# Kernel tuning notes

Hardware: AMD Instinct MI355X
Metric: run time of the kernel (lower is better)

Reference implementation:

```python
import jax, jax.numpy as jnp
import numpy as np

GAMMAK = 1.0 / 256.0  # 1/(2*d) so kernel values don't underflow for unit-gaussian data


def setup_inputs() -> dict:
    key = jax.random.key(0)
    k1, k2, k3, k4, k5 = jax.random.split(key, 5)
    N, d = 8192, 128
    X = jax.random.normal(k1, (N, d), dtype=jnp.float32)
    y = jax.random.normal(k2, (N - 1, d), dtype=jnp.float32)
    y_next = jax.random.normal(k3, (N - 1, d), dtype=jnp.float32)
    # reset_transform initializes R=eye, t=0; perturb slightly for nontrivial math
    R = jnp.eye(d, dtype=jnp.float32) + 0.01 * jax.random.normal(k4, (d, d), dtype=jnp.float32)
    t = 0.01 * jax.random.normal(k5, (d, 1), dtype=jnp.float32)
    return {"X": X, "y": y, "y_next": y_next, "R": R, "t": t}


def reference(X, y, y_next, R, t):
    # _transform_pts: (R @ y.T + t).T == y @ R.T + t.squeeze()
    yt = y @ R.T + t[:, 0]            # (N-1, d)
    Xb = X[:-1]                        # (N-1, d) kernel base points
    # pairwise_sqeuclidean(Xb, yt), clamped at 0
    sq = jnp.clip(
        jnp.sum(Xb * Xb, axis=1)[:, None]
        + jnp.sum(yt * yt, axis=1)[None, :]
        - 2.0 * (Xb @ yt.T),
        0.0, None,
    )                                  # (N-1, N-1)
    G = jnp.exp(-GAMMAK * sq)
    # diag(1/rowsum) @ G  ==  G / rowsum[:, None]  (avoids explicit NxN diagonal)
    y_pred = (G / jnp.sum(G, axis=1, keepdims=True)) @ X[1:]  # (N-1, d)
    return y_pred
```

## Files before the change

### kernel.cpp

```cpp
#include <hip/hip_runtime.h>
#include <hip/hip_bf16.h>


#define LOG2E 1.44269504088896340736f
#define KNEG (-(1.0f/256.0f)*LOG2E)
#define KA2C (2.0f*(1.0f/256.0f)*LOG2E)

typedef __attribute__((ext_vector_type(4)))  float f32x4;
typedef __attribute__((ext_vector_type(16))) float f32x16;
typedef __attribute__((ext_vector_type(8)))  short bf16x8;

__device__ __forceinline__ unsigned short f2bf(float f) {
  unsigned u = __builtin_bit_cast(unsigned, f);
  u = (u + 0x7fffu + ((u >> 16) & 1u)) >> 16;
  return (unsigned short)u;
}
__device__ __forceinline__ unsigned pk2bf(float a, float b) {
  __hip_bfloat162 h = __float22bfloat162_rn(float2{a, b});
  unsigned u;
  __builtin_memcpy(&u, &h, 4);
  return u;
}
__device__ __forceinline__ bf16x8 pack8(float4 p0, float4 p1) {
  uint4 u;
  u.x = pk2bf(p0.x, p0.y); u.y = pk2bf(p0.z, p0.w);
  u.z = pk2bf(p1.x, p1.y); u.w = pk2bf(p1.z, p1.w);
  return __builtin_bit_cast(bf16x8, u);
}
__device__ __forceinline__ float fast_exp2(float x) {
#if __has_builtin(__builtin_amdgcn_exp2f)
  return __builtin_amdgcn_exp2f(x);
#else
  return exp2f(x);
#endif
}
__device__ __forceinline__ void gl2lds16(const void* g, void* l) {
  __builtin_amdgcn_global_load_lds((const __attribute__((address_space(1))) unsigned int*)g,
                                   (__attribute__((address_space(3))) unsigned int*)l, 16, 0, 0);
}
__device__ __forceinline__ f32x16 mfma_32x32x16(bf16x8 a, bf16x8 b, f32x16 c) {
  return __builtin_amdgcn_mfma_f32_32x32x16_bf16(a, b, c, 0, 0, 0);
}

#define T32S  16384
#define V32O  8192

__global__ __launch_bounds__(256) void k_prep(const float* __restrict__ y,
                                              const float* __restrict__ R,
                                              const float* __restrict__ t,
                                              const float* __restrict__ X,
                                              unsigned short* __restrict__ ctp,
                                              float* __restrict__ ynp) {
  __shared__ union {
    unsigned short ytt[128 * 132];
    float xt[65 * 132];
  } sm;
  const int tid = threadIdx.x;

  if (blockIdx.x < 64) {
    const int wv = tid >> 6, ln = tid & 63;
    const int l = ln & 31, h = ln >> 5;
    const int B = blockIdx.x;
    const int rw = B * 128 + wv * 32;

    bf16x8 af[8];
    {
      int row = rw + l; if (row > 8190) row = 8190;
      const float* yr = y + (size_t)row * 128;
#pragma unroll
      for (int kc = 0; kc < 8; ++kc) {
        float4 p0 = *(const float4*)(yr + kc*16 + 8*h);
        float4 p1 = *(const float4*)(yr + kc*16 + 8*h + 4);
        af[kc] = pack8(p0, p1);
      }
    }
    f32x16 acc[4];
#pragma unroll
    for (int cc=0; cc<4; ++cc)
#pragma unroll
      for (int i=0;i<16;++i) acc[cc][i] = 0.f;
#pragma unroll
    for (int cc=0; cc<4; ++cc) {
      const float* Rr = R + (size_t)(cc*32 + l) * 128;
#pragma unroll
      for (int kc=0; kc<8; ++kc) {
        float4 p0 = *(const float4*)(Rr + kc*16 + 8*h);
        float4 p1 = *(const float4*)(Rr + kc*16 + 8*h + 4);
        acc[cc] = mfma_32x32x16(af[kc], pack8(p0, p1), acc[cc]);
      }
    }
    float tv0 = t[l], tv1 = t[32+l], tv2 = t[64+l], tv3 = t[96+l];
    float v0[16], v1[16], v2[16], v3[16], ssq[16];
#pragma unroll
    for (int r=0;r<16;++r) {
      v0[r]=acc[0][r]+tv0; v1[r]=acc[1][r]+tv1; v2[r]=acc[2][r]+tv2; v3[r]=acc[3][r]+tv3;
      ssq[r] = v0[r]*v0[r] + v1[r]*v1[r] + v2[r]*v2[r] + v3[r]*v3[r];
    }
#pragma unroll
    for (int off=1; off<32; off<<=1)
#pragma unroll
      for (int r=0;r<16;++r) ssq[r] += __shfl_xor(ssq[r], off, 64);
    if (l < 16) {
      int r = l;
      int grow = rw + (r&3) + 8*(r>>2) + 4*h;
      ynp[grow] = (grow >= 8191) ? -1.0e30f : KNEG * ssq[r];
    }
#pragma unroll
    for (int r=0;r<16;++r) {
      int rloc = wv*32 + (r&3) + 8*(r>>2) + 4*h;
      sm.ytt[rloc*132 +   0 + l] = f2bf(KA2C * v0[r]);
      sm.ytt[rloc*132 +  32 + l] = f2bf(KA2C * v1[r]);
      sm.ytt[rloc*132 +  64 + l] = f2bf(KA2C * v2[r]);
      sm.ytt[rloc*132 +  96 + l] = f2bf(KA2C * v3[r]);
    }
    __syncthreads();
    const int Tt = B*4 + wv;
    char* base = (char*)ctp + (size_t)Tt*T32S;
#pragma unroll
    for (int kc=0;kc<8;++kc) {
      const unsigned short* s = &sm.ytt[(wv*32 + l)*132 + kc*16 + 8*h];
      uint2 a = *(const uint2*)(s);
      uint2 b = *(const uint2*)(s + 4);
      uint4 o; o.x=a.x; o.y=a.y; o.z=b.x; o.w=b.y;
      *(uint4*)(base + kc*1024 + ln*16) = o;
    }
  } else {
    const int T = blockIdx.x - 64;
    const int jt = T * 64;
    {
      int rr = tid >> 2, q4 = tid & 3;
      int row = jt + rr; if (row > 8191) row = 8191;
      const float* src = X + (size_t)row*128 + q4*32;
      float* dst = &sm.xt[rr*132 + q4*32];
#pragma unroll
      for (int i=0;i<8;++i) *(float4*)(dst + i*4) = *(const float4*)(src + i*4);
      if (tid < 4) {
        int row2 = jt + 64; if (row2 > 8191) row2 = 8191;
        const float* s2 = X + (size_t)row2*128 + tid*32;
        float* d2 = &sm.xt[64*132 + tid*32];
#pragma unroll
        for (int i=0;i<8;++i) *(float4*)(d2 + i*4) = *(const float4*)(s2 + i*4);
      }
    }
    __syncthreads();
#pragma unroll
    for (int it=0; it<4; ++it) {
      int E = tid + it*256;
      int lp = E & 63, grp = E >> 6;
      int cc = grp & 3, jc16 = grp >> 2;
      int jb = jc16*16 + 8*(lp>>5);
      int c  = cc*32 + (lp & 31);
      uint4 o;
      o.x = pk2bf(sm.xt[(jb+1)*132 + c], sm.xt[(jb+2)*132 + c]);
      o.y = pk2bf(sm.xt[(jb+3)*132 + c], sm.xt[(jb+4)*132 + c]);
      o.z = pk2bf(sm.xt[(jb+5)*132 + c], sm.xt[(jb+6)*132 + c]);
      o.w = pk2bf(sm.xt[(jb+7)*132 + c], sm.xt[(jb+8)*132 + c]);
      int t32 = T*2 + (jc16 >> 1);
      int chunk = (jc16 & 1)*4 + cc;
      *(uint4*)((char*)ctp + (size_t)t32*T32S + V32O + chunk*1024 + lp*16) = o;
    }
  }
}

__global__ __launch_bounds__(256, 3) void k_main(
    const float* __restrict__ X,
    const unsigned short* __restrict__ ctp,
    const float* __restrict__ ynp,
    float* __restrict__ accp,
    float* __restrict__ rsp,
    int js) {
  __shared__ unsigned short stg[2][T32S/2];
  __shared__ unsigned short gls[4*32*68];
  const int tid = threadIdx.x;
  const int wv = tid >> 6, ln = tid & 63;
  const int l = ln & 31, h = ln >> 5;
  const int row = blockIdx.x*128 + wv*32 + l;

  bf16x8 qf[8];
  {
    const float* xr = X + (size_t)row * 128;
#pragma unroll
    for (int kc=0;kc<8;++kc) {
      float4 p0 = *(const float4*)(xr + kc*16 + 8*h);
      float4 p1 = *(const float4*)(xr + kc*16 + 8*h + 4);
      qf[kc] = pack8(p0, p1);
    }
  }
  f32x16 acc[4];
#pragma unroll
  for (int cc=0;cc<4;++cc)
#pragma unroll
    for (int i=0;i<16;++i) acc[cc][i]=0.f;
  float rs = 0.f;
  const int sp = blockIdx.y;
  const int Tbeg = (sp * 256) / js;
  const int Tend = ((sp + 1) * 256) / js;

  {
    const char* cb = (const char*)ctp + (size_t)Tbeg*T32S;
#pragma unroll
    for (int i=0;i<4;++i) {
      int c = wv*4 + i;
      gl2lds16(cb + c*1024 + ln*16, (char*)stg[0] + c*1024);
    }
  }
  int cur = 0;
  for (int T = Tbeg; T < Tend; ++T) {
    __syncthreads();
    if (T + 1 < Tend) {
      const char* cb = (const char*)ctp + (size_t)(T+1)*T32S;
#pragma unroll
      for (int i=0;i<4;++i) {
        int c = wv*4 + i;
        gl2lds16(cb + c*1024 + ln*16, (char*)stg[cur^1] + c*1024);
      }
    }
    const char* yb = (const char*)stg[cur];
    const char* vb = (const char*)stg[cur] + V32O;
    f32x4 yv[4];
#pragma unroll
    for (int rg=0;rg<4;++rg)
      yv[rg] = *(const f32x4*)(ynp + T*32 + 8*rg + 4*h);
    f32x16 s0, s1;
#pragma unroll
    for (int i=0;i<16;++i) { s0[i]=0.f; s1[i]=0.f; }
#pragma unroll
    for (int kc=0;kc<4;++kc) {
      bf16x8 a0 = *(const bf16x8*)(yb + (2*kc  )*1024 + ln*16);
      bf16x8 a1 = *(const bf16x8*)(yb + (2*kc+1)*1024 + ln*16);
      s0 = mfma_32x32x16(a0, qf[2*kc  ], s0);
      s1 = mfma_32x32x16(a1, qf[2*kc+1], s1);
    }
#pragma unroll
    for (int rg=0;rg<4;++rg) {
      float g0 = fast_exp2(s0[rg*4+0] + s1[rg*4+0] + yv[rg][0]);
      float g1 = fast_exp2(s0[rg*4+1] + s1[rg*4+1] + yv[rg][1]);
      float g2 = fast_exp2(s0[rg*4+2] + s1[rg*4+2] + yv[rg][2]);
      float g3 = fast_exp2(s0[rg*4+3] + s1[rg*4+3] + yv[rg][3]);
      rs += (g0+g1) + (g2+g3);
      uint2 w; w.x = pk2bf(g0, g1); w.y = pk2bf(g2, g3);
      int j0 = 8*rg + 4*h;
      *(uint2*)&gls[(wv*32+l)*68 + j0] = w;
    }
    __builtin_amdgcn_wave_barrier();
#pragma unroll
    for (int jj=0; jj<2; ++jj) {
      const unsigned short* gp = &gls[(wv*32+l)*68 + jj*16 + 8*h];
      uint2 g0 = *(const uint2*)(gp);
      uint2 g1 = *(const uint2*)(gp + 4);
      uint4 gv; gv.x=g0.x; gv.y=g0.y; gv.z=g1.x; gv.w=g1.y;
      bf16x8 pb = __builtin_bit_cast(bf16x8, gv);
#pragma unroll
      for (int cc=0;cc<4;++cc) {
        bf16x8 a2 = *(const bf16x8*)(vb + (jj*4+cc)*1024 + ln*16);
        acc[cc] = mfma_32x32x16(a2, pb, acc[cc]);
      }
    }
    __builtin_amdgcn_wave_barrier();
    cur ^= 1;
  }
  rs += __shfl_xor(rs, 32, 64);
  if (h == 0) rsp[(size_t)sp*8192 + row] = rs;
#pragma unroll
  for (int cc=0;cc<4;++cc)
#pragma unroll
    for (int r=0;r<16;++r) {
      int c = cc*32 + (r&3) + 8*(r>>2) + 4*h;
      accp[((size_t)sp*128 + c)*8192 + row] = acc[cc][r];
    }
}

__global__ __launch_bounds__(256) void k_fin(const float* __restrict__ accp,
                                             const float* __restrict__ rsp,
                                             float* __restrict__ out,
                                             int js) {
  __shared__ float tr[64*68];
  __shared__ float rinv[64];
  const int tid = threadIdx.x;
  const int r0 = blockIdx.x * 64;
  const int c0 = blockIdx.y * 64;
  if (tid < 64) {
    float s = 0.f;
    for (int sp=0; sp<js; ++sp) s += rsp[(size_t)sp*8192 + r0 + tid];
    rinv[tid] = 1.f / s;
  }
  const int rq = tid & 15, cg = tid >> 4;
  float v[4][4];
#pragma unroll
  for (int cc=0;cc<4;++cc)
#pragma unroll
    for (int k=0;k<4;++k) v[cc][k]=0.f;
  for (int sp=0; sp<js; ++sp) {
    const float* base = accp + ((size_t)sp*128 + c0 + cg*4)*8192 + r0 + rq*4;
#pragma unroll
    for (int cc=0; cc<4; ++cc) {
      float4 p = *(const float4*)(base + (size_t)cc*8192);
      v[cc][0]+=p.x; v[cc][1]+=p.y; v[cc][2]+=p.z; v[cc][3]+=p.w;
    }
  }
  __syncthreads();
#pragma unroll
  for (int cc=0;cc<4;++cc)
#pragma unroll
    for (int k=0;k<4;++k)
      tr[(rq*4+k)*68 + cg*4+cc] = v[cc][k] * rinv[rq*4+k];
  __syncthreads();
  {
    int r = tid >> 2, q = tid & 3;
    int grow = r0 + r;
    if (grow < 8191) {
      float* dst = out + (size_t)grow*128 + c0 + q*16;
      const float* s2 = &tr[r*68 + q*16];
#pragma unroll
      for (int i=0;i<4;++i) *(float4*)(dst + i*4) = *(const float4*)(s2 + i*4);
    }
  }
}

extern "C" void kernel_launch(void* const* d_in, const int* in_sizes, int n_in,
                              void* d_out, int out_size, void* d_ws, size_t ws_size,
                              hipStream_t stream) {
  const float* X = (const float*)d_in[0];
  const float* y = (const float*)d_in[1];
  const float* R = (const float*)d_in[3];
  const float* t = (const float*)d_in[4];
  float* out = (float*)d_out;
  char* ws = (char*)d_ws;

  unsigned short* ctp = (unsigned short*)ws;
  size_t ynoff = (size_t)256 * T32S;
  float* ynp = (float*)(ws + ynoff);
  size_t rspoff = ynoff + 32*1024;
  float* rsp  = (float*)(ws + rspoff);
  size_t accoff = rspoff + 512*1024;
  float* accp = (float*)(ws + accoff);

  int js = 12;
  while (js > 1 && accoff + (size_t)js*128*8192*4 > ws_size) js >>= 1;

  k_prep<<<dim3(192), dim3(256), 0, stream>>>(y, R, t, X, ctp, ynp);
  k_main<<<dim3(64, js), dim3(256), 0, stream>>>(X, ctp, ynp, accp, rsp, js);
  k_fin<<<dim3(128, 2), dim3(256), 0, stream>>>(accp, rsp, out, js);
}
```

Measured before the change: 139.7 us.

## Process two 32-row query groups per wave to reuse staged Y/V tiles

Each wave now holds query fragments and accumulators for two 32-row groups, 128 rows apart. Every LDS-staged Y and V fragment feeds two MFMAs instead of one, which halves LDS and global tile traffic per output row. The two score accumulators, which used to split the K dimension, now belong to separate row groups. The grid shrinks to 32 row blocks, the column split goes from 12 to 16, and the occupancy hint drops from 3 to 2 blocks per CU to make room for the doubled register and LDS footprint. The risks are fewer resident waves to hide latency and a longer MFMA dependency chain per accumulator.

```diff
diff --git a/kernel.cpp b/kernel.cpp
--- a/kernel.cpp
+++ b/kernel.cpp
@@ -162,7 +162,7 @@
   }
 }
 
-__global__ __launch_bounds__(256, 3) void k_main(
+__global__ __launch_bounds__(256, 2) void k_main(
     const float* __restrict__ X,
     const unsigned short* __restrict__ ctp,
     const float* __restrict__ ynp,
@@ -170,28 +170,31 @@
     float* __restrict__ rsp,
     int js) {
   __shared__ unsigned short stg[2][T32S/2];
-  __shared__ unsigned short gls[4*32*68];
+  __shared__ unsigned short gls[2*4*32*68];
   const int tid = threadIdx.x;
   const int wv = tid >> 6, ln = tid & 63;
   const int l = ln & 31, h = ln >> 5;
-  const int row = blockIdx.x*128 + wv*32 + l;
-
-  bf16x8 qf[8];
-  {
-    const float* xr = X + (size_t)row * 128;
+  const int rbase = blockIdx.x*256 + wv*32;
+
+  bf16x8 qf[2][8];
+#pragma unroll
+  for (int g=0; g<2; ++g) {
+    const float* xr = X + (size_t)(rbase + g*128 + l) * 128;
 #pragma unroll
     for (int kc=0;kc<8;++kc) {
       float4 p0 = *(const float4*)(xr + kc*16 + 8*h);
       float4 p1 = *(const float4*)(xr + kc*16 + 8*h + 4);
-      qf[kc] = pack8(p0, p1);
-    }
-  }
-  f32x16 acc[4];
-#pragma unroll
-  for (int cc=0;cc<4;++cc)
-#pragma unroll
-    for (int i=0;i<16;++i) acc[cc][i]=0.f;
-  float rs = 0.f;
+      qf[g][kc] = pack8(p0, p1);
+    }
+  }
+  f32x16 acc[2][4];
+#pragma unroll
+  for (int g=0;g<2;++g)
+#pragma unroll
+    for (int cc=0;cc<4;++cc)
+#pragma unroll
+      for (int i=0;i<16;++i) acc[g][cc][i]=0.f;
+  float rs0 = 0.f, rs1 = 0.f;
   const int sp = blockIdx.y;
   const int Tbeg = (sp * 256) / js;
   const int Tend = ((sp + 1) * 256) / js;
@@ -217,57 +220,73 @@
     }
     const char* yb = (const char*)stg[cur];
     const char* vb = (const char*)stg[cur] + V32O;
-    f32x4 yv[4];
-#pragma unroll
-    for (int rg=0;rg<4;++rg)
-      yv[rg] = *(const f32x4*)(ynp + T*32 + 8*rg + 4*h);
     f32x16 s0, s1;
 #pragma unroll
     for (int i=0;i<16;++i) { s0[i]=0.f; s1[i]=0.f; }
 #pragma unroll
-    for (int kc=0;kc<4;++kc) {
-      bf16x8 a0 = *(const bf16x8*)(yb + (2*kc  )*1024 + ln*16);
-      bf16x8 a1 = *(const bf16x8*)(yb + (2*kc+1)*1024 + ln*16);
-      s0 = mfma_32x32x16(a0, qf[2*kc  ], s0);
-      s1 = mfma_32x32x16(a1, qf[2*kc+1], s1);
+    for (int kc=0;kc<8;++kc) {
+      bf16x8 a = *(const bf16x8*)(yb + kc*1024 + ln*16);
+      s0 = mfma_32x32x16(a, qf[0][kc], s0);
+      s1 = mfma_32x32x16(a, qf[1][kc], s1);
     }
 #pragma unroll
     for (int rg=0;rg<4;++rg) {
-      float g0 = fast_exp2(s0[rg*4+0] + s1[rg*4+0] + yv[rg][0]);
-      float g1 = fast_exp2(s0[rg*4+1] + s1[rg*4+1] + yv[rg][1]);
-      float g2 = fast_exp2(s0[rg*4+2] + s1[rg*4+2] + yv[rg][2]);
-      float g3 = fast_exp2(s0[rg*4+3] + s1[rg*4+3] + yv[rg][3]);
-      rs += (g0+g1) + (g2+g3);
-      uint2 w; w.x = pk2bf(g0, g1); w.y = pk2bf(g2, g3);
-      int j0 = 8*rg + 4*h;
-      *(uint2*)&gls[(wv*32+l)*68 + j0] = w;
+      f32x4 yv = *(const f32x4*)(ynp + T*32 + 8*rg + 4*h);
+      {
+        float g0 = fast_exp2(s0[rg*4+0] + yv[0]);
+        float g1 = fast_exp2(s0[rg*4+1] + yv[1]);
+        float g2 = fast_exp2(s0[rg*4+2] + yv[2]);
+        float g3 = fast_exp2(s0[rg*4+3] + yv[3]);
+        rs0 += (g0+g1) + (g2+g3);
+        uint2 w; w.x = pk2bf(g0, g1); w.y = pk2bf(g2, g3);
+        *(uint2*)&gls[(wv*32+l)*68 + 8*rg + 4*h] = w;
+      }
+      {
+        float g0 = fast_exp2(s1[rg*4+0] + yv[0]);
+        float g1 = fast_exp2(s1[rg*4+1] + yv[1]);
+        float g2 = fast_exp2(s1[rg*4+2] + yv[2]);
+        float g3 = fast_exp2(s1[rg*4+3] + yv[3]);
+        rs1 += (g0+g1) + (g2+g3);
+        uint2 w; w.x = pk2bf(g0, g1); w.y = pk2bf(g2, g3);
+        *(uint2*)&gls[((4+wv)*32+l)*68 + 8*rg + 4*h] = w;
+      }
     }
     __builtin_amdgcn_wave_barrier();
 #pragma unroll
     for (int jj=0; jj<2; ++jj) {
-      const unsigned short* gp = &gls[(wv*32+l)*68 + jj*16 + 8*h];
-      uint2 g0 = *(const uint2*)(gp);
-      uint2 g1 = *(const uint2*)(gp + 4);
-      uint4 gv; gv.x=g0.x; gv.y=g0.y; gv.z=g1.x; gv.w=g1.y;
-      bf16x8 pb = __builtin_bit_cast(bf16x8, gv);
+      const unsigned short* gp0 = &gls[(wv*32+l)*68 + jj*16 + 8*h];
+      const unsigned short* gp1 = &gls[((4+wv)*32+l)*68 + jj*16 + 8*h];
+      uint2 a0 = *(const uint2*)(gp0); uint2 b0 = *(const uint2*)(gp0 + 4);
+      uint2 a1 = *(const uint2*)(gp1); uint2 b1 = *(const uint2*)(gp1 + 4);
+      uint4 u0; u0.x=a0.x; u0.y=a0.y; u0.z=b0.x; u0.w=b0.y;
+      uint4 u1; u1.x=a1.x; u1.y=a1.y; u1.z=b1.x; u1.w=b1.y;
+      bf16x8 pb0 = __builtin_bit_cast(bf16x8, u0);
+      bf16x8 pb1 = __builtin_bit_cast(bf16x8, u1);
 #pragma unroll
       for (int cc=0;cc<4;++cc) {
         bf16x8 a2 = *(const bf16x8*)(vb + (jj*4+cc)*1024 + ln*16);
-        acc[cc] = mfma_32x32x16(a2, pb, acc[cc]);
+        acc[0][cc] = mfma_32x32x16(a2, pb0, acc[0][cc]);
+        acc[1][cc] = mfma_32x32x16(a2, pb1, acc[1][cc]);
       }
     }
     __builtin_amdgcn_wave_barrier();
     cur ^= 1;
   }
-  rs += __shfl_xor(rs, 32, 64);
-  if (h == 0) rsp[(size_t)sp*8192 + row] = rs;
-#pragma unroll
-  for (int cc=0;cc<4;++cc)
-#pragma unroll
-    for (int r=0;r<16;++r) {
-      int c = cc*32 + (r&3) + 8*(r>>2) + 4*h;
-      accp[((size_t)sp*128 + c)*8192 + row] = acc[cc][r];
-    }
+  rs0 += __shfl_xor(rs0, 32, 64);
+  rs1 += __shfl_xor(rs1, 32, 64);
+  if (h == 0) {
+    rsp[(size_t)sp*8192 + rbase + l] = rs0;
+    rsp[(size_t)sp*8192 + rbase + 128 + l] = rs1;
+  }
+#pragma unroll
+  for (int g=0;g<2;++g)
+#pragma unroll
+    for (int cc=0;cc<4;++cc)
+#pragma unroll
+      for (int r=0;r<16;++r) {
+        int c = cc*32 + (r&3) + 8*(r>>2) + 4*h;
+        accp[((size_t)sp*128 + c)*8192 + rbase + g*128 + l] = acc[g][cc][r];
+      }
 }
 
 __global__ __launch_bounds__(256) void k_fin(const float* __restrict__ accp,
@@ -332,13 +351,13 @@
   float* ynp = (float*)(ws + ynoff);
   size_t rspoff = ynoff + 32*1024;
   float* rsp  = (float*)(ws + rspoff);
-  size_t accoff = rspoff + 512*1024;
+  size_t accoff = rspoff + 1024*1024;
   float* accp = (float*)(ws + accoff);
 
-  int js = 12;
+  int js = 16;
   while (js > 1 && accoff + (size_t)js*128*8192*4 > ws_size) js >>= 1;
 
   k_prep<<<dim3(192), dim3(256), 0, stream>>>(y, R, t, X, ctp, ynp);
-  k_main<<<dim3(64, js), dim3(256), 0, stream>>>(X, ctp, ynp, accp, rsp, js);
+  k_main<<<dim3(32, js), dim3(256), 0, stream>>>(X, ctp, ynp, accp, rsp, js);
   k_fin<<<dim3(128, 2), dim3(256), 0, stream>>>(accp, rsp, out, js);
 }
```

Result: slower. 146.2 us (+4.6%).
